# Performance work log

Measured on AMD Instinct MI355X. Metric: run time of the kernel, lower is better.

Reference implementation:

```python
import jax, jax.numpy as jnp
import numpy as np

N, C, H, W = 16, 512, 64, 64
C_BAR, C_HAT = 64, 256


def max_pool2(t):
    # t: [n, c, h, w] -> [n, c, h//2, w//2] via 2x2 max pool
    n, c, h, w = t.shape
    return t.reshape(n, c, h // 2, 2, w // 2, 2).max(axis=(3, 5))


def setup_inputs() -> dict:
    key = jax.random.key(0)
    ks = jax.random.split(key, 6)
    x = jax.random.normal(ks[0], (N, C, H, W), dtype=jnp.float32)
    # 1x1 conv weights stored as [out_channels, in_channels]
    w_theta = jax.random.normal(ks[1], (C_BAR, C), dtype=jnp.float32) * 0.02
    w_phi = jax.random.normal(ks[2], (C_BAR, C), dtype=jnp.float32) * 0.02
    w_g = jax.random.normal(ks[3], (C_HAT, C), dtype=jnp.float32) * 0.02
    w_o = jax.random.normal(ks[4], (C, C_HAT), dtype=jnp.float32) * 0.02
    # gamma initialized to zero in the module; use a small nonzero value so the
    # attention path contributes to the output (and to gradients).
    gamma = jnp.full((1,), 0.1, dtype=jnp.float32)
    return {"x": x, "w_theta": w_theta, "w_phi": w_phi, "w_g": w_g,
            "w_o": w_o, "gamma": gamma}


def reference(x, w_theta, w_phi, w_g, w_o, gamma):
    n, c, h, w = x.shape
    hw, hw4 = h * w, (h * w) // 4
    # 1x1 conv projections (pure channel GEMMs)
    g_x = jnp.einsum('nchw,oc->nohw', x, w_g)          # [n, c_hat, h, w]
    g_x = max_pool2(g_x).reshape(n, -1, hw4)            # [n, c_hat, hw/4]
    phi_x = jnp.einsum('nchw,oc->nohw', x, w_phi)       # [n, c_bar, h, w]
    phi_x = max_pool2(phi_x).reshape(n, -1, hw4)        # [n, c_bar, hw/4]
    theta_x = jnp.einsum('nchw,oc->nohw', x, w_theta).reshape(n, -1, hw)  # [n, c_bar, hw]
    # bmm -> softmax -> bmm
    scores = jnp.einsum('nds,ndt->nst', theta_x, phi_x)  # [n, hw, hw/4]
    attn = jax.nn.softmax(scores, axis=-1)
    y = jnp.einsum('ndt,nst->nds', g_x, attn)            # [n, c_hat, hw]
    y = y.reshape(n, -1, h, w)
    o = jnp.einsum('nchw,oc->nohw', y, w_o)              # [n, c, h, w]
    return gamma[0] * o + x
```

## Files before the change

kernel.cpp:

```cpp
#include <hip/hip_runtime.h>
#include <stdint.h>

typedef unsigned short u16;
typedef u16   us4 __attribute__((ext_vector_type(4)));
typedef u16   us8 __attribute__((ext_vector_type(8)));
typedef __bf16 bf8 __attribute__((ext_vector_type(8)));
typedef float f4  __attribute__((ext_vector_type(4)));

__device__ __forceinline__ u16 f2bf(float f) {
    uint32_t u = __builtin_bit_cast(uint32_t, f);
    uint32_t r = (u + 0x7fffu + ((u >> 16) & 1u)) >> 16;
    return (u16)r;
}
__device__ __forceinline__ float bf2f(u16 s) {
    uint32_t u = ((uint32_t)s) << 16;
    return __builtin_bit_cast(float, u);
}
__device__ __forceinline__ u16 cvtbf(float f) {
    return __builtin_bit_cast(u16, (__bf16)f);
}
__device__ __forceinline__ f4 mfma16(bf8 a, bf8 b, f4 c) {
    return __builtin_amdgcn_mfma_f32_16x16x32_bf16(a, b, c, 0, 0, 0);
}
__device__ __forceinline__ u16 max4bf(u16 a, u16 b, u16 c, u16 d) {
    float m = fmaxf(fmaxf(bf2f(a), bf2f(b)), fmaxf(bf2f(c), bf2f(d)));
    return f2bf(m);
}

__global__ __launch_bounds__(256) void xt_kernel(
    const float* __restrict__ x, u16* __restrict__ Xt)
{
    const int s0 = blockIdx.x * 64, c0 = blockIdx.y * 64, n = blockIdx.z;
    const int tid = threadIdx.x;
    __shared__ u16 lds[64 * 72];

    {
        int c_loc = tid & 63, s_seg = (tid >> 6) * 16;
        const float* src = x + ((size_t)n * 512 + c0 + c_loc) * 4096 + s0 + s_seg;
        for (int i4 = 0; i4 < 4; i4++) {
            float4 f = *(const float4*)(src + i4 * 4);
            int s = s_seg + i4 * 4;
            lds[(s + 0) * 72 + c_loc] = f2bf(f.x);
            lds[(s + 1) * 72 + c_loc] = f2bf(f.y);
            lds[(s + 2) * 72 + c_loc] = f2bf(f.z);
            lds[(s + 3) * 72 + c_loc] = f2bf(f.w);
        }
    }
    __syncthreads();
    {
        int s_loc = tid >> 2, c_seg = (tid & 3) * 16;
        u16* dst = Xt + ((size_t)n * 4096 + s0 + s_loc) * 512 + c0 + c_seg;
        *(us8*)(dst)     = *(const us8*)&lds[s_loc * 72 + c_seg];
        *(us8*)(dst + 8) = *(const us8*)&lds[s_loc * 72 + c_seg + 8];
    }
}

__global__ __launch_bounds__(256) void wconv_kernel(
    const float* __restrict__ w_theta, const float* __restrict__ w_phi,
    const float* __restrict__ w_g, const float* __restrict__ w_o,
    u16* __restrict__ Wall_bf, u16* __restrict__ Wo_bf)
{
    int base = (blockIdx.x * 256 + threadIdx.x) * 4;
    const float* src; u16* dst;
    if (base < 32768)       { src = w_theta + base;          dst = Wall_bf + base; }
    else if (base < 65536)  { src = w_phi + (base - 32768);  dst = Wall_bf + base; }
    else if (base < 196608) { src = w_g + (base - 65536);    dst = Wall_bf + base; }
    else                    { src = w_o + (base - 196608);   dst = Wo_bf + (base - 196608); }
    float4 f = *(const float4*)src;
    us4 v; v[0] = f2bf(f.x); v[1] = f2bf(f.y); v[2] = f2bf(f.z); v[3] = f2bf(f.w);
    *(us4*)dst = v;
}

__global__ __launch_bounds__(256) void projT_gemm(
    const u16* __restrict__ Xt, const u16* __restrict__ Wall_bf,
    u16* __restrict__ PT)
{
    const int s0 = blockIdx.x * 128;
    const int r0 = blockIdx.y * 128;
    const int nb = blockIdx.z;
    const int tid = threadIdx.x;
    const int wave = tid >> 6, lane = tid & 63;
    const int quad = lane >> 4, l15 = lane & 15;
    const int wm = (wave >> 1) * 64, wn = (wave & 1) * 64;

    __shared__ u16 a_lds[128 * 40];
    __shared__ u16 b_lds[128 * 40];

    f4 acc[4][4];
    f4 z = {0.f, 0.f, 0.f, 0.f};
    for (int i = 0; i < 4; i++) for (int j = 0; j < 4; j++) acc[i][j] = z;

    const u16* Abase = Xt + ((size_t)nb * 4096 + s0) * 512;
    const int m = tid >> 1, kseg = (tid & 1) * 16;

    for (int k0 = 0; k0 < 512; k0 += 32) {
        *(us8*)&a_lds[m * 40 + kseg]     = *(const us8*)(Abase + (size_t)m * 512 + k0 + kseg);
        *(us8*)&a_lds[m * 40 + kseg + 8] = *(const us8*)(Abase + (size_t)m * 512 + k0 + kseg + 8);
        *(us8*)&b_lds[m * 40 + kseg]     = *(const us8*)(Wall_bf + (size_t)(r0 + m) * 512 + k0 + kseg);
        *(us8*)&b_lds[m * 40 + kseg + 8] = *(const us8*)(Wall_bf + (size_t)(r0 + m) * 512 + k0 + kseg + 8);
        __syncthreads();
        bf8 af[4], bfr[4];
        for (int i = 0; i < 4; i++)
            af[i]  = __builtin_bit_cast(bf8, *(const us8*)&a_lds[(wm + i*16 + l15)*40 + quad*8]);
        for (int j = 0; j < 4; j++)
            bfr[j] = __builtin_bit_cast(bf8, *(const us8*)&b_lds[(wn + j*16 + l15)*40 + quad*8]);
        for (int i = 0; i < 4; i++)
            for (int j = 0; j < 4; j++)
                acc[i][j] = mfma16(af[i], bfr[j], acc[i][j]);
        __syncthreads();
    }
    for (int i = 0; i < 4; i++) {
        int s_idx = s0 + wm + i * 16 + quad * 4;
        for (int rr = 0; rr < 4; rr++) {
            u16* dst = PT + ((size_t)nb * 4096 + s_idx + rr) * 384 + r0 + wn + l15;
            for (int j = 0; j < 4; j++)
                dst[j * 16] = f2bf(acc[i][j][rr]);
        }
    }
}

__global__ __launch_bounds__(256) void phi_pool2(
    const u16* __restrict__ PT, u16* __restrict__ phiF)
{
    int n = blockIdx.y, t0 = blockIdx.x * 64;
    int tid = threadIdx.x;
    int t_loc = tid >> 2, d0 = (tid & 3) * 16;
    int t = t0 + t_loc;
    int h2 = t >> 5, w2 = t & 31;
    int s00 = h2 * 128 + w2 * 2;
    const u16* base = PT + ((size_t)n * 4096) * 384 + 64 + d0;
    us8 r[4][2];
    int soff[4] = {s00, s00 + 1, s00 + 64, s00 + 65};
    for (int p = 0; p < 4; p++) {
        r[p][0] = *(const us8*)(base + (size_t)soff[p] * 384);
        r[p][1] = *(const us8*)(base + (size_t)soff[p] * 384 + 8);
    }
    us8 o0, o1;
    for (int i = 0; i < 8; i++) {
        o0[i] = max4bf(r[0][0][i], r[1][0][i], r[2][0][i], r[3][0][i]);
        o1[i] = max4bf(r[0][1][i], r[1][1][i], r[2][1][i], r[3][1][i]);
    }
    size_t fb = (((size_t)n * 32 + (t >> 5)) * 2 + ((t >> 4) & 1)) * 1024
              + (size_t)(d0 >> 5) * 512
              + (size_t)(((d0 >> 3) & 3) * 16 + (t & 15)) * 8;
    *(us8*)(phiF + fb)       = o0;
    *(us8*)(phiF + fb + 128) = o1;
}

__global__ __launch_bounds__(256) void g_poolT(
    const u16* __restrict__ PT, u16* __restrict__ gF)
{
    int t0 = blockIdx.x * 64, d0 = blockIdx.y * 64, n = blockIdx.z;
    int tid = threadIdx.x;
    __shared__ u16 lds[64 * 72];

    {
        int t_loc = tid & 63, dseg = (tid >> 6) * 16;
        int t = t0 + t_loc;
        int h2 = t >> 5, w2 = t & 31;
        int s00 = h2 * 128 + w2 * 2;
        const u16* base = PT + ((size_t)n * 4096) * 384 + 128 + d0 + dseg;
        us8 r[4][2];
        int soff[4] = {s00, s00 + 1, s00 + 64, s00 + 65};
        for (int p = 0; p < 4; p++) {
            r[p][0] = *(const us8*)(base + (size_t)soff[p] * 384);
            r[p][1] = *(const us8*)(base + (size_t)soff[p] * 384 + 8);
        }
        for (int i = 0; i < 8; i++) {
            lds[(dseg + i) * 72 + t_loc]     = max4bf(r[0][0][i], r[1][0][i], r[2][0][i], r[3][0][i]);
            lds[(dseg + 8 + i) * 72 + t_loc] = max4bf(r[0][1][i], r[1][1][i], r[2][1][i], r[3][1][i]);
        }
    }
    __syncthreads();
    {
        int d_loc = tid >> 2, t_seg = (tid & 3) * 16;
        size_t fb = ((((size_t)n * 4 + blockIdx.y) * 4 + (d_loc >> 4)) * 32
                     + (t0 >> 5) + (t_seg >> 5)) * 512
                  + (size_t)((((t_seg >> 3) & 3)) * 16 + (d_loc & 15)) * 8;
        *(us8*)(gF + fb)       = *(const us8*)&lds[d_loc * 72 + t_seg];
        *(us8*)(gF + fb + 128) = *(const us8*)&lds[d_loc * 72 + t_seg + 8];
    }
}

__global__ __launch_bounds__(512, 4) void attn_kernel(
    const u16* __restrict__ PT, const u16* __restrict__ phiF,
    const u16* __restrict__ gF, u16* __restrict__ yT)
{
    const int orig = blockIdx.x;
    const int tile = (orig & 7) * 64 + (orig >> 3);
    const int n = tile >> 5;
    const int q0b = (tile & 31) * 128;

    const int tid = threadIdx.x;
    const int wave = tid >> 6, lane = tid & 63, quad = lane >> 4, l15 = lane & 15;

    __shared__ u16 p_lds[2][8][16 * 40];
    __shared__ u16 phi_lds[2][32 * 72];
    __shared__ float qsum[128];

    const u16* th = PT + ((size_t)n * 4096 + q0b + wave * 16 + l15) * 384 + quad * 8;
    bf8 bth0 = __builtin_bit_cast(bf8, *(const us8*)(th));
    bf8 bth1 = __builtin_bit_cast(bf8, *(const us8*)(th + 32));

    const u16* gbase = gF + ((size_t)n * 16 + wave * 2) * 16384 + lane * 8;

    const u16* phi_src = phiF + (size_t)n * 65536 + tid * 4;
    const int sl = (tid >> 1) & 63;
    const int st = ((tid >> 8) & 1) * 16 + (sl & 15);
    const int sd = ((tid >> 7) & 1) * 32 + (sl >> 4) * 8 + (tid & 1) * 4;
    u16* pdst0 = &phi_lds[0][st * 72 + sd];
    u16* pdst1 = &phi_lds[1][st * 72 + sd];

    f4 z = {0.f, 0.f, 0.f, 0.f};
    f4 acc[2][8];
    for (int i = 0; i < 2; i++) for (int j = 0; j < 8; j++) acc[i][j] = z;
    float lsum = 0.f;

    {
        us4 p0 = *(const us4*)(phi_src);
        *(us4*)pdst0 = p0;
    }
    us4 pf = *(const us4*)(phi_src + 2048);
    us8 gg0 = *(const us8*)(gbase);
    us8 gg1 = *(const us8*)(gbase + 16384);
    __syncthreads();

    for (int ci = 0; ci < 32; ci++) {
        const int buf = ci & 1;
        const u16* pl  = buf ? phi_lds[1] : phi_lds[0];
        u16* pbw = buf ? &p_lds[1][0][0] : &p_lds[0][0][0];

        for (int tt = 0; tt < 2; tt++) {
            bf8 ap0 = __builtin_bit_cast(bf8, *(const us8*)&pl[(tt * 16 + l15) * 72 + quad * 8]);
            bf8 ap1 = __builtin_bit_cast(bf8, *(const us8*)&pl[(tt * 16 + l15) * 72 + 32 + quad * 8]);
            f4 s = mfma16(ap0, bth0, z);
            s = mfma16(ap1, bth1, s);
            us4 pk; float ps = 0.f;
            for (int rr = 0; rr < 4; rr++) {
                float p = __expf(s[rr]);
                ps += p;
                pk[rr] = cvtbf(p);
            }
            lsum += ps;
            *(us4*)&pbw[wave * 640 + l15 * 40 + tt * 16 + quad * 4] = pk;
        }

        *(us4*)(buf ? pdst0 : pdst1) = pf;

        __syncthreads();

        us8 ggn0, ggn1;
        {
            const int c2 = (ci + 2 < 32) ? ci + 2 : 31;
            pf = *(const us4*)(phi_src + (size_t)c2 * 2048);
            const int c1 = (ci + 1 < 32) ? ci + 1 : 31;
            ggn0 = *(const us8*)(gbase + (size_t)c1 * 512);
            ggn1 = *(const us8*)(gbase + 16384 + (size_t)c1 * 512);
        }

        bf8 ag0 = __builtin_bit_cast(bf8, gg0);
        bf8 ag1 = __builtin_bit_cast(bf8, gg1);
        const u16* pbr = buf ? &p_lds[1][0][0] : &p_lds[0][0][0];
        for (int j = 0; j < 8; j++) {
            bf8 bp = __builtin_bit_cast(bf8, *(const us8*)&pbr[j * 640 + l15 * 40 + quad * 8]);
            acc[0][j] = mfma16(ag0, bp, acc[0][j]);
            acc[1][j] = mfma16(ag1, bp, acc[1][j]);
        }
        gg0 = ggn0; gg1 = ggn1;
    }

    float v = lsum;
    v += __shfl_xor(v, 16);
    v += __shfl_xor(v, 32);
    if (lane < 16) qsum[wave * 16 + lane] = v;
    __syncthreads();

    for (int j = 0; j < 8; j++) {
        float invj = 1.0f / qsum[j * 16 + l15];
        u16* dst = yT + ((size_t)n * 4096 + q0b + j * 16 + l15) * 256 + wave * 32 + quad * 4;
        for (int i = 0; i < 2; i++) {
            us4 o;
            for (int rr = 0; rr < 4; rr++) o[rr] = cvtbf(acc[i][j][rr] * invj);
            *(us4*)(dst + i * 16) = o;
        }
    }
}

__global__ __launch_bounds__(256) void oproj_gemm(
    const u16* __restrict__ Wo_bf, const u16* __restrict__ yT,
    const float* __restrict__ x, const float* __restrict__ gamma,
    float* __restrict__ out)
{
    const int nt = blockIdx.x;
    const int mt = blockIdx.y;
    const int nb = blockIdx.z;
    const int tid = threadIdx.x;
    const int wave = tid >> 6, lane = tid & 63;
    const int quad = lane >> 4, l15 = lane & 15;
    const int wm = (wave >> 1) * 32, wn = (wave & 1) * 64;
    const int s0 = nt * 128;

    __shared__ u16 a_lds[64 * 40];
    __shared__ u16 b_lds[128 * 40];

    f4 acc[2][4];
    f4 z = {0.f, 0.f, 0.f, 0.f};
    for (int i = 0; i < 2; i++) for (int j = 0; j < 4; j++) acc[i][j] = z;

    for (int k0 = 0; k0 < 256; k0 += 32) {
        {
            int m = tid >> 2, kq = (tid & 3) * 8;
            *(us8*)&a_lds[m * 40 + kq] =
                *(const us8*)(Wo_bf + (size_t)(mt * 64 + m) * 256 + k0 + kq);
        }
        {
            int s_loc = tid >> 1, kq = (tid & 1) * 16;
            const u16* src = yT + ((size_t)nb * 4096 + s0 + s_loc) * 256 + k0 + kq;
            *(us8*)&b_lds[s_loc * 40 + kq]     = *(const us8*)(src);
            *(us8*)&b_lds[s_loc * 40 + kq + 8] = *(const us8*)(src + 8);
        }
        __syncthreads();
        bf8 af[2], bfr[4];
        for (int i = 0; i < 2; i++)
            af[i] = __builtin_bit_cast(bf8, *(const us8*)&a_lds[(wm + i*16 + l15)*40 + quad*8]);
        for (int j = 0; j < 4; j++)
            bfr[j] = __builtin_bit_cast(bf8, *(const us8*)&b_lds[(wn + j*16 + l15)*40 + quad*8]);
        for (int i = 0; i < 2; i++)
            for (int j = 0; j < 4; j++)
                acc[i][j] = mfma16(af[i], bfr[j], acc[i][j]);
        __syncthreads();
    }
    float g0 = gamma[0];
    for (int i = 0; i < 2; i++) {
        int c = mt * 64 + wm + i * 16 + quad * 4;
        for (int j = 0; j < 4; j++) {
            int s = s0 + wn + j * 16 + l15;
            for (int rr = 0; rr < 4; rr++) {
                size_t idx = ((size_t)nb * 512 + c + rr) * 4096 + s;
                out[idx] = g0 * acc[i][j][rr] + x[idx];
            }
        }
    }
}

extern "C" void kernel_launch(void* const* d_in, const int* in_sizes, int n_in,
                              void* d_out, int out_size, void* d_ws, size_t ws_size,
                              hipStream_t stream)
{
    (void)in_sizes; (void)n_in; (void)out_size; (void)ws_size;
    const float* x       = (const float*)d_in[0];
    const float* w_theta = (const float*)d_in[1];
    const float* w_phi   = (const float*)d_in[2];
    const float* w_g     = (const float*)d_in[3];
    const float* w_o     = (const float*)d_in[4];
    const float* gamma   = (const float*)d_in[5];
    float* out = (float*)d_out;

    char* ws = (char*)d_ws;
    u16* Xt      = (u16*)(ws);
    u16* yT      = (u16*)(ws);
    u16* phiF    = (u16*)(ws + 33554432);
    u16* gF      = (u16*)(ws + 35651584);
    u16* Wall_bf = (u16*)(ws + 67108864);
    u16* Wo_bf   = (u16*)(ws + 67502080);
    u16* PT      = (u16*)(ws + 67764224);

    xt_kernel  <<<dim3(64, 8, 16), 256, 0, stream>>>(x, Xt);
    wconv_kernel<<<320, 256, 0, stream>>>(w_theta, w_phi, w_g, w_o, Wall_bf, Wo_bf);
    projT_gemm <<<dim3(32, 3, 16), 256, 0, stream>>>(Xt, Wall_bf, PT);
    phi_pool2  <<<dim3(16, 16),    256, 0, stream>>>(PT, phiF);
    g_poolT    <<<dim3(16, 4, 16), 256, 0, stream>>>(PT, gF);
    attn_kernel<<<dim3(512),       512, 0, stream>>>(PT, phiF, gF, yT);
    oproj_gemm <<<dim3(32, 8, 16), 256, 0, stream>>>(Wo_bf, yT, x, gamma, out);
}
```

Baseline: 405.2 us.

## Double-buffer LDS and register-prefetch global tiles in projection and output GEMMs

Both the projection GEMM and the output-projection GEMM now keep two LDS buffers and prefetch the next K-slice from global memory into registers while MFMAs run on the current buffer. This cuts the loop from two barriers per iteration to one and lets global load latency overlap with compute. The cost is double the LDS footprint and extra live registers, which may reduce occupancy. The last iterations reload a clamped slice redundantly.

```diff
diff --git a/kernel.cpp b/kernel.cpp
--- a/kernel.cpp
+++ b/kernel.cpp
@@ -83,31 +83,49 @@
     const int quad = lane >> 4, l15 = lane & 15;
     const int wm = (wave >> 1) * 64, wn = (wave & 1) * 64;
 
-    __shared__ u16 a_lds[128 * 40];
-    __shared__ u16 b_lds[128 * 40];
+    __shared__ u16 a_lds[2][128 * 40];
+    __shared__ u16 b_lds[2][128 * 40];
 
     f4 acc[4][4];
     f4 z = {0.f, 0.f, 0.f, 0.f};
     for (int i = 0; i < 4; i++) for (int j = 0; j < 4; j++) acc[i][j] = z;
 
-    const u16* Abase = Xt + ((size_t)nb * 4096 + s0) * 512;
     const int m = tid >> 1, kseg = (tid & 1) * 16;
-
-    for (int k0 = 0; k0 < 512; k0 += 32) {
-        *(us8*)&a_lds[m * 40 + kseg]     = *(const us8*)(Abase + (size_t)m * 512 + k0 + kseg);
-        *(us8*)&a_lds[m * 40 + kseg + 8] = *(const us8*)(Abase + (size_t)m * 512 + k0 + kseg + 8);
-        *(us8*)&b_lds[m * 40 + kseg]     = *(const us8*)(Wall_bf + (size_t)(r0 + m) * 512 + k0 + kseg);
-        *(us8*)&b_lds[m * 40 + kseg + 8] = *(const us8*)(Wall_bf + (size_t)(r0 + m) * 512 + k0 + kseg + 8);
-        __syncthreads();
+    const u16* As = Xt + ((size_t)nb * 4096 + s0 + m) * 512 + kseg;
+    const u16* Bs = Wall_bf + (size_t)(r0 + m) * 512 + kseg;
+
+    {
+        us8 x0 = *(const us8*)(As), x1 = *(const us8*)(As + 8);
+        us8 y0 = *(const us8*)(Bs), y1 = *(const us8*)(Bs + 8);
+        *(us8*)&a_lds[0][m * 40 + kseg]     = x0;
+        *(us8*)&a_lds[0][m * 40 + kseg + 8] = x1;
+        *(us8*)&b_lds[0][m * 40 + kseg]     = y0;
+        *(us8*)&b_lds[0][m * 40 + kseg + 8] = y1;
+    }
+    us8 pa0 = *(const us8*)(As + 32), pa1 = *(const us8*)(As + 40);
+    us8 pb0 = *(const us8*)(Bs + 32), pb1 = *(const us8*)(Bs + 40);
+    __syncthreads();
+
+    for (int ci = 0; ci < 16; ci++) {
+        const int buf = ci & 1;
         bf8 af[4], bfr[4];
         for (int i = 0; i < 4; i++)
-            af[i]  = __builtin_bit_cast(bf8, *(const us8*)&a_lds[(wm + i*16 + l15)*40 + quad*8]);
+            af[i]  = __builtin_bit_cast(bf8, *(const us8*)&a_lds[buf][(wm + i*16 + l15)*40 + quad*8]);
         for (int j = 0; j < 4; j++)
-            bfr[j] = __builtin_bit_cast(bf8, *(const us8*)&b_lds[(wn + j*16 + l15)*40 + quad*8]);
+            bfr[j] = __builtin_bit_cast(bf8, *(const us8*)&b_lds[buf][(wn + j*16 + l15)*40 + quad*8]);
         for (int i = 0; i < 4; i++)
             for (int j = 0; j < 4; j++)
                 acc[i][j] = mfma16(af[i], bfr[j], acc[i][j]);
+        *(us8*)&a_lds[buf ^ 1][m * 40 + kseg]     = pa0;
+        *(us8*)&a_lds[buf ^ 1][m * 40 + kseg + 8] = pa1;
+        *(us8*)&b_lds[buf ^ 1][m * 40 + kseg]     = pb0;
+        *(us8*)&b_lds[buf ^ 1][m * 40 + kseg + 8] = pb1;
         __syncthreads();
+        const int k2 = ((ci + 2 < 16) ? ci + 2 : 15) * 32;
+        pa0 = *(const us8*)(As + k2);
+        pa1 = *(const us8*)(As + k2 + 8);
+        pb0 = *(const us8*)(Bs + k2);
+        pb1 = *(const us8*)(Bs + k2 + 8);
     }
     for (int i = 0; i < 4; i++) {
         int s_idx = s0 + wm + i * 16 + quad * 4;
@@ -300,35 +318,47 @@
     const int wm = (wave >> 1) * 32, wn = (wave & 1) * 64;
     const int s0 = nt * 128;
 
-    __shared__ u16 a_lds[64 * 40];
-    __shared__ u16 b_lds[128 * 40];
+    __shared__ u16 a_lds[2][64 * 40];
+    __shared__ u16 b_lds[2][128 * 40];
 
     f4 acc[2][4];
     f4 z = {0.f, 0.f, 0.f, 0.f};
     for (int i = 0; i < 2; i++) for (int j = 0; j < 4; j++) acc[i][j] = z;
 
-    for (int k0 = 0; k0 < 256; k0 += 32) {
-        {
-            int m = tid >> 2, kq = (tid & 3) * 8;
-            *(us8*)&a_lds[m * 40 + kq] =
-                *(const us8*)(Wo_bf + (size_t)(mt * 64 + m) * 256 + k0 + kq);
-        }
-        {
-            int s_loc = tid >> 1, kq = (tid & 1) * 16;
-            const u16* src = yT + ((size_t)nb * 4096 + s0 + s_loc) * 256 + k0 + kq;
-            *(us8*)&b_lds[s_loc * 40 + kq]     = *(const us8*)(src);
-            *(us8*)&b_lds[s_loc * 40 + kq + 8] = *(const us8*)(src + 8);
-        }
-        __syncthreads();
+    const int ma = tid >> 2, kqa = (tid & 3) * 8;
+    const int mb = tid >> 1, kqb = (tid & 1) * 16;
+    const u16* As = Wo_bf + (size_t)(mt * 64 + ma) * 256 + kqa;
+    const u16* Bs = yT + ((size_t)nb * 4096 + s0 + mb) * 256 + kqb;
+
+    {
+        us8 a0 = *(const us8*)(As);
+        us8 b0 = *(const us8*)(Bs), b1 = *(const us8*)(Bs + 8);
+        *(us8*)&a_lds[0][ma * 40 + kqa]     = a0;
+        *(us8*)&b_lds[0][mb * 40 + kqb]     = b0;
+        *(us8*)&b_lds[0][mb * 40 + kqb + 8] = b1;
+    }
+    us8 pa = *(const us8*)(As + 32);
+    us8 pb0 = *(const us8*)(Bs + 32), pb1 = *(const us8*)(Bs + 40);
+    __syncthreads();
+
+    for (int ci = 0; ci < 8; ci++) {
+        const int buf = ci & 1;
         bf8 af[2], bfr[4];
         for (int i = 0; i < 2; i++)
-            af[i] = __builtin_bit_cast(bf8, *(const us8*)&a_lds[(wm + i*16 + l15)*40 + quad*8]);
+            af[i] = __builtin_bit_cast(bf8, *(const us8*)&a_lds[buf][(wm + i*16 + l15)*40 + quad*8]);
         for (int j = 0; j < 4; j++)
-            bfr[j] = __builtin_bit_cast(bf8, *(const us8*)&b_lds[(wn + j*16 + l15)*40 + quad*8]);
+            bfr[j] = __builtin_bit_cast(bf8, *(const us8*)&b_lds[buf][(wn + j*16 + l15)*40 + quad*8]);
         for (int i = 0; i < 2; i++)
             for (int j = 0; j < 4; j++)
                 acc[i][j] = mfma16(af[i], bfr[j], acc[i][j]);
+        *(us8*)&a_lds[buf ^ 1][ma * 40 + kqa]     = pa;
+        *(us8*)&b_lds[buf ^ 1][mb * 40 + kqb]     = pb0;
+        *(us8*)&b_lds[buf ^ 1][mb * 40 + kqb + 8] = pb1;
         __syncthreads();
+        const int k2 = ((ci + 2 < 8) ? ci + 2 : 7) * 32;
+        pa  = *(const us8*)(As + k2);
+        pb0 = *(const us8*)(Bs + k2);
+        pb1 = *(const us8*)(Bs + k2 + 8);
     }
     float g0 = gamma[0];
     for (int i = 0; i < 2; i++) {
```

Measured after the change: 393.8 us, median of 2. 1.03x faster.
